# Optimization experiments

Hardware: AMD Instinct MI355X
Metric: run time of the kernel (lower is better)

## Reference

```python
import jax, jax.numpy as jnp
import numpy as np
from jax import lax

STRIDE = 1
PADDING = 1


def setup_inputs() -> dict:
    key = jax.random.key(0)
    k1, k2 = jax.random.split(key)
    x = jax.random.normal(k1, (32, 128, 56, 56), dtype=jnp.float32)
    weight = jax.random.normal(k2, (256, 128, 3, 3), dtype=jnp.float32)
    bias = jnp.zeros((256,), dtype=jnp.float32)
    return {"x": x, "weight": weight, "bias": bias}


def reference(x, weight, bias):
    # Standard 2D cross-correlation (the intended math of the torch
    # unfold + broadcast-multiply + sum implementation):
    #   out[b,o,h,w] = sum_{i,kh,kw} x_pad[b,i,h*s+kh,w*s+kw] * weight[o,i,kh,kw] + bias[o]
    out = lax.conv_general_dilated(
        x, weight,
        window_strides=(STRIDE, STRIDE),
        padding=[(PADDING, PADDING), (PADDING, PADDING)],
        dimension_numbers=("NCHW", "OIHW", "NCHW"),
    )
    return out + bias[None, :, None, None]
```

## Files before the change

kernel.cpp:

```cpp
#include <hip/hip_runtime.h>
#include <cstdint>
#include <cstddef>

#define NB    32
#define CI    128
#define CO    256
#define HW_   56
#define HP    58
#define KTOT  1152
#define NKT   36
#define MTOT  (NB * HW_ * HW_)

static constexpr size_t XP_ELEMS = (size_t)NB * HP * HP * CI;
static constexpr size_t WT_ELEMS = (size_t)CO * KTOT;
static constexpr size_t XP_BYTES = XP_ELEMS * 2;
static constexpr size_t WT_BYTES = WT_ELEMS * 2;

typedef __attribute__((ext_vector_type(8))) short bf16x8;
typedef __attribute__((ext_vector_type(4))) float f32x4;

__device__ __forceinline__ short f32_to_bf16(float f) {
  uint32_t u = __float_as_uint(f);
  uint32_t r = (u + 0x7FFFu + ((u >> 16) & 1u)) >> 16;
  return (short)r;
}

typedef __attribute__((address_space(3))) void       lds_void;
typedef const __attribute__((address_space(1))) void gbl_void;

__device__ __forceinline__ void gload16(const void* g, void* l) {
  __builtin_amdgcn_global_load_lds((gbl_void*)g, (lds_void*)l, 16, 0, 0);
}

__global__ void pad_convert(const float* __restrict__ x, short* __restrict__ xp,
                            const float* __restrict__ wt, short* __restrict__ wbT) {
  __shared__ float lds[CI][57];
  const int blk = blockIdx.x;
  const int hp  = blk % HP;
  const int nb  = blk / HP;
  const int tid = threadIdx.x;

  if (blk < 1152) {
    int idx = blk * 256 + tid;
    int c  = idx & 127;
    int t  = idx >> 7;
    int kw = t % 3;  int t2 = t / 3;
    int kh = t2 % 3; int o  = t2 / 3;
    wbT[idx] = f32_to_bf16(wt[(((size_t)o * CI + c) * 3 + kh) * 3 + kw]);
  }

  const bool interior = (hp >= 1 && hp <= HW_);
  if (interior) {
    const float* src = x + (size_t)nb * CI * HW_ * HW_ + (size_t)(hp - 1) * HW_;
    for (int t = tid; t < CI * HW_; t += 256) {
      int c = t / HW_, w = t - (t / HW_) * HW_;
      lds[c][w] = src[(size_t)c * HW_ * HW_ + w];
    }
  }
  __syncthreads();
  short* dst = xp + (size_t)(nb * HP + hp) * HP * CI;
  for (int t = tid; t < HP * CI / 4; t += 256) {
    const int wp = t >> 5;
    const int c4 = (t & 31) * 4;
    short4 s;
    if (interior && wp >= 1 && wp <= HW_) {
      s.x = f32_to_bf16(lds[c4 + 0][wp - 1]);
      s.y = f32_to_bf16(lds[c4 + 1][wp - 1]);
      s.z = f32_to_bf16(lds[c4 + 2][wp - 1]);
      s.w = f32_to_bf16(lds[c4 + 3][wp - 1]);
    } else {
      s.x = s.y = s.z = s.w = 0;
    }
    *(short4*)(dst + t * 4) = s;
  }
}

__device__ __forceinline__ int stage_aoff(int u) {
  const int tap = u >> 2;
  const int cq  = u & 3;
  const int kh  = tap / 3, kw = tap - kh * 3;
  return ((kh * HP + kw) * CI + cq * 32) * 2;
}

__global__ __launch_bounds__(256, 2) void conv_gemm(
    const short* __restrict__ xp, const short* __restrict__ wbT,
    const float* __restrict__ bias, float* __restrict__ out) {
  __shared__ __align__(16) char lds_[3 * 24576];

  const int tid = threadIdx.x;
  const int l   = tid & 63;
  const int wv  = tid >> 6;
  const int wm  = wv >> 1;
  const int wn  = wv & 1;

  const int bid = blockIdx.x;
  const int lin = (bid & 7) * 98 + (bid >> 3);
  const int mt  = lin >> 1;
  const int nt  = lin & 1;

  const int pcs = (((l & 3) ^ ((l >> 3) & 3)) << 4);
  const int srow = 16 * wv + (l >> 2);
  const char *aSrc0, *aSrc1, *aSrc2, *aSrc3;
  {
#pragma unroll
    for (int g = 0; g < 4; ++g) {
      int m  = mt * 256 + 64 * g + srow;
      int nb = m / 3136, hw = m - nb * 3136;
      int h = hw / HW_, w = hw - (hw / HW_) * HW_;
      const char* p = (const char*)xp + ((size_t)((nb * HP + h) * HP + w) * CI) * 2 + pcs;
      if (g == 0) aSrc0 = p; else if (g == 1) aSrc1 = p;
      else if (g == 2) aSrc2 = p; else aSrc3 = p;
    }
  }
  const char* bSrc0 = (const char*)wbT + (size_t)(nt * 128 +      srow) * KTOT * 2 + pcs;
  const char* bSrc1 = (const char*)wbT + (size_t)(nt * 128 + 64 + srow) * KTOT * 2 + pcs;

  const int lm   = l & 15;
  const int koff = (((l >> 4) ^ ((l >> 1) & 3)) << 4);
  const int raOff = (wm * 128 + lm) * 64 + koff;
  const int rbOff = (wn * 64 + lm) * 64 + koff;

  char* B0 = lds_;
  char* B1 = lds_ + 24576;
  char* B2 = lds_ + 49152;

#define STAGE(U, BUF)                                                        \
  {                                                                          \
    const int ao_ = stage_aoff(U);                                           \
    const int bo_ = (U) * 64;                                                \
    gload16(aSrc0 + ao_, (BUF) +         wv * 1024);                         \
    gload16(aSrc1 + ao_, (BUF) +  4096 + wv * 1024);                         \
    gload16(aSrc2 + ao_, (BUF) +  8192 + wv * 1024);                         \
    gload16(aSrc3 + ao_, (BUF) + 12288 + wv * 1024);                         \
    gload16(bSrc0 + bo_, (BUF) + 16384 + wv * 1024);                         \
    gload16(bSrc1 + bo_, (BUF) + 20480 + wv * 1024);                         \
  }

  f32x4 acc[8][4];
#pragma unroll
  for (int g = 0; g < 8; ++g)
#pragma unroll
    for (int h = 0; h < 4; ++h) acc[g][h] = {0.f, 0.f, 0.f, 0.f};

  STAGE(0, B0)
  STAGE(1, B1)
  asm volatile("s_waitcnt vmcnt(6)" ::: "memory");
  __builtin_amdgcn_s_barrier();
  __builtin_amdgcn_sched_barrier(0);

#define TILE_BODY(V, CUR, STG)                                               \
  {                                                                          \
    const int v_ = (V);                                                      \
    if (v_ + 2 < NKT) STAGE(v_ + 2, STG)                                     \
    bf16x8 af[8], bf[4];                                                     \
    _Pragma("unroll") for (int g = 0; g < 8; ++g)                            \
        af[g] = *(const bf16x8*)((CUR) + raOff + g * 1024);                  \
    _Pragma("unroll") for (int h = 0; h < 4; ++h)                            \
        bf[h] = *(const bf16x8*)((CUR) + 16384 + rbOff + h * 1024);          \
    __builtin_amdgcn_s_setprio(1);                                           \
    _Pragma("unroll") for (int g = 0; g < 8; ++g)                            \
      _Pragma("unroll") for (int h = 0; h < 4; ++h)                          \
        acc[g][h] = __builtin_amdgcn_mfma_f32_16x16x32_bf16(                 \
            bf[h], af[g], acc[g][h], 0, 0, 0);                               \
    __builtin_amdgcn_s_setprio(0);                                           \
    if (v_ < NKT - 1) {                                                      \
      if (v_ == NKT - 2) { asm volatile("s_waitcnt vmcnt(0)" ::: "memory"); }\
      else               { asm volatile("s_waitcnt vmcnt(6)" ::: "memory"); }\
      __builtin_amdgcn_s_barrier();                                          \
      __builtin_amdgcn_sched_barrier(0);                                     \
    }                                                                        \
  }

  for (int v3 = 0; v3 < NKT; v3 += 3) {
    TILE_BODY(v3 + 0, B0, B2)
    TILE_BODY(v3 + 1, B1, B0)
    TILE_BODY(v3 + 2, B2, B1)
  }
#undef TILE_BODY
#undef STAGE

  const int mBase = mt * 256 + wm * 128 + lm;
  const int ocB   = nt * 128 + wn * 64 + (l >> 4) * 4;
  float bv[4][4];
#pragma unroll
  for (int h = 0; h < 4; ++h)
#pragma unroll
    for (int j = 0; j < 4; ++j) bv[h][j] = bias[ocB + h * 16 + j];
#pragma unroll
  for (int g = 0; g < 8; ++g) {
    const int m  = mBase + g * 16;
    const int nb = m / 3136;
    const int hw = m - nb * 3136;
    float* op = out + (size_t)nb * CO * 3136 + hw;
#pragma unroll
    for (int h = 0; h < 4; ++h) {
      const int oc = ocB + h * 16;
#pragma unroll
      for (int j = 0; j < 4; ++j)
        op[(size_t)(oc + j) * 3136] = acc[g][h][j] + bv[h][j];
    }
  }
}

__global__ void conv_naive(const float* __restrict__ x, const float* __restrict__ wt,
                           const float* __restrict__ bias, float* __restrict__ out) {
  const int idx = blockIdx.x * 256 + threadIdx.x;
  if (idx >= NB * CO * 3136) return;
  const int w  = idx % HW_;
  const int h  = (idx / HW_) % HW_;
  const int oc = (idx / 3136) % CO;
  const int nb = idx / (3136 * CO);
  float s = bias[oc];
  for (int c = 0; c < CI; ++c)
    for (int kh = 0; kh < 3; ++kh) {
      const int ih = h + kh - 1;
      if (ih < 0 || ih >= HW_) continue;
      for (int kw = 0; kw < 3; ++kw) {
        const int iw = w + kw - 1;
        if (iw < 0 || iw >= HW_) continue;
        s += x[((size_t)(nb * CI + c) * HW_ + ih) * HW_ + iw] *
             wt[(((size_t)oc * CI + c) * 3 + kh) * 3 + kw];
      }
    }
  out[idx] = s;
}

extern "C" void kernel_launch(void* const* d_in, const int* in_sizes, int n_in,
                              void* d_out, int out_size, void* d_ws, size_t ws_size,
                              hipStream_t stream) {
  const float* x    = (const float*)d_in[0];
  const float* wt   = (const float*)d_in[1];
  const float* bias = (const float*)d_in[2];
  float* out        = (float*)d_out;

  if (ws_size < XP_BYTES + WT_BYTES) {
    conv_naive<<<(NB * CO * 3136 + 255) / 256, 256, 0, stream>>>(x, wt, bias, out);
    return;
  }

  short* xp  = (short*)d_ws;
  short* wbT = (short*)((char*)d_ws + XP_BYTES);

  pad_convert<<<NB * HP, 256, 0, stream>>>(x, xp, wt, wbT);
  conv_gemm<<<(MTOT / 256) * 2, 256, 0, stream>>>(xp, wbT, bias, out);
}
```

Measured before the change: 94.21 us.

## Enlarge conv GEMM block tile to 256x256 with 8 waves and split-phase staging

```diff
diff --git a/kernel.cpp b/kernel.cpp
--- a/kernel.cpp
+++ b/kernel.cpp
@@ -82,38 +82,35 @@
   return ((kh * HP + kw) * CI + cq * 32) * 2;
 }
 
-__global__ __launch_bounds__(256, 2) void conv_gemm(
+__global__ __launch_bounds__(512, 2) void conv_gemm(
     const short* __restrict__ xp, const short* __restrict__ wbT,
     const float* __restrict__ bias, float* __restrict__ out) {
-  __shared__ __align__(16) char lds_[3 * 24576];
+  __shared__ __align__(16) char lds_[3 * 32768];
 
   const int tid = threadIdx.x;
   const int l   = tid & 63;
   const int wv  = tid >> 6;
-  const int wm  = wv >> 1;
-  const int wn  = wv & 1;
+  const int wm  = wv >> 2;
+  const int wn  = wv & 3;
 
   const int bid = blockIdx.x;
-  const int lin = (bid & 7) * 98 + (bid >> 3);
-  const int mt  = lin >> 1;
-  const int nt  = lin & 1;
-
-  const int pcs = (((l & 3) ^ ((l >> 3) & 3)) << 4);
-  const int srow = 16 * wv + (l >> 2);
-  const char *aSrc0, *aSrc1, *aSrc2, *aSrc3;
+  const int mt  = (bid & 7) * 49 + (bid >> 3);
+
+  const int pcs  = (((tid & 3) ^ ((tid >> 3) & 3)) << 4);
+  const int srow = tid >> 2;
+  const char *aSrc0, *aSrc1;
   {
 #pragma unroll
-    for (int g = 0; g < 4; ++g) {
-      int m  = mt * 256 + 64 * g + srow;
+    for (int q = 0; q < 2; ++q) {
+      int m  = mt * 256 + 128 * q + srow;
       int nb = m / 3136, hw = m - nb * 3136;
       int h = hw / HW_, w = hw - (hw / HW_) * HW_;
       const char* p = (const char*)xp + ((size_t)((nb * HP + h) * HP + w) * CI) * 2 + pcs;
-      if (g == 0) aSrc0 = p; else if (g == 1) aSrc1 = p;
-      else if (g == 2) aSrc2 = p; else aSrc3 = p;
-    }
-  }
-  const char* bSrc0 = (const char*)wbT + (size_t)(nt * 128 +      srow) * KTOT * 2 + pcs;
-  const char* bSrc1 = (const char*)wbT + (size_t)(nt * 128 + 64 + srow) * KTOT * 2 + pcs;
+      if (q == 0) aSrc0 = p; else aSrc1 = p;
+    }
+  }
+  const char* bSrc0 = (const char*)wbT + (size_t)(      srow) * KTOT * 2 + pcs;
+  const char* bSrc1 = (const char*)wbT + (size_t)(128 + srow) * KTOT * 2 + pcs;
 
   const int lm   = l & 15;
   const int koff = (((l >> 4) ^ ((l >> 1) & 3)) << 4);
@@ -121,19 +118,20 @@
   const int rbOff = (wn * 64 + lm) * 64 + koff;
 
   char* B0 = lds_;
-  char* B1 = lds_ + 24576;
-  char* B2 = lds_ + 49152;
-
-#define STAGE(U, BUF)                                                        \
+  char* B1 = lds_ + 32768;
+  char* B2 = lds_ + 65536;
+
+#define STAGE_A(U, BUF)                                                      \
   {                                                                          \
     const int ao_ = stage_aoff(U);                                           \
+    gload16(aSrc0 + ao_, (BUF) +        wv * 1024);                          \
+    gload16(aSrc1 + ao_, (BUF) + 8192 + wv * 1024);                          \
+  }
+#define STAGE_B(U, BUF)                                                      \
+  {                                                                          \
     const int bo_ = (U) * 64;                                                \
-    gload16(aSrc0 + ao_, (BUF) +         wv * 1024);                         \
-    gload16(aSrc1 + ao_, (BUF) +  4096 + wv * 1024);                         \
-    gload16(aSrc2 + ao_, (BUF) +  8192 + wv * 1024);                         \
-    gload16(aSrc3 + ao_, (BUF) + 12288 + wv * 1024);                         \
     gload16(bSrc0 + bo_, (BUF) + 16384 + wv * 1024);                         \
-    gload16(bSrc1 + bo_, (BUF) + 20480 + wv * 1024);                         \
+    gload16(bSrc1 + bo_, (BUF) + 24576 + wv * 1024);                         \
   }
 
   f32x4 acc[8][4];
@@ -142,32 +140,55 @@
 #pragma unroll
     for (int h = 0; h < 4; ++h) acc[g][h] = {0.f, 0.f, 0.f, 0.f};
 
-  STAGE(0, B0)
-  STAGE(1, B1)
-  asm volatile("s_waitcnt vmcnt(6)" ::: "memory");
+  STAGE_A(0, B0) STAGE_B(0, B0)
+  STAGE_A(1, B1) STAGE_B(1, B1)
+  asm volatile("s_waitcnt vmcnt(4)" ::: "memory");
   __builtin_amdgcn_s_barrier();
   __builtin_amdgcn_sched_barrier(0);
 
 #define TILE_BODY(V, CUR, STG)                                               \
   {                                                                          \
     const int v_ = (V);                                                      \
-    if (v_ + 2 < NKT) STAGE(v_ + 2, STG)                                     \
-    bf16x8 af[8], bf[4];                                                     \
-    _Pragma("unroll") for (int g = 0; g < 8; ++g)                            \
-        af[g] = *(const bf16x8*)((CUR) + raOff + g * 1024);                  \
-    _Pragma("unroll") for (int h = 0; h < 4; ++h)                            \
-        bf[h] = *(const bf16x8*)((CUR) + 16384 + rbOff + h * 1024);          \
-    __builtin_amdgcn_s_setprio(1);                                           \
-    _Pragma("unroll") for (int g = 0; g < 8; ++g)                            \
+    bf16x8 bf[4];                                                            \
+                                         \
+    if (v_ + 2 < NKT) STAGE_A(v_ + 2, STG)                                   \
+    {                                                                        \
+      bf16x8 af[4];                                                          \
+      _Pragma("unroll") for (int g = 0; g < 4; ++g)                          \
+          af[g] = *(const bf16x8*)((CUR) + raOff + g * 1024);                \
       _Pragma("unroll") for (int h = 0; h < 4; ++h)                          \
-        acc[g][h] = __builtin_amdgcn_mfma_f32_16x16x32_bf16(                 \
-            bf[h], af[g], acc[g][h], 0, 0, 0);                               \
-    __builtin_amdgcn_s_setprio(0);                                           \
-    if (v_ < NKT - 1) {                                                      \
-      if (v_ == NKT - 2) { asm volatile("s_waitcnt vmcnt(0)" ::: "memory"); }\
-      else               { asm volatile("s_waitcnt vmcnt(6)" ::: "memory"); }\
-      __builtin_amdgcn_s_barrier();                                          \
-      __builtin_amdgcn_sched_barrier(0);                                     \
+          bf[h] = *(const bf16x8*)((CUR) + 16384 + rbOff + h * 1024);        \
+      __builtin_amdgcn_s_barrier();                                          \
+      asm volatile("s_waitcnt lgkmcnt(0)" ::: "memory");                     \
+      __builtin_amdgcn_sched_barrier(0);                                     \
+      __builtin_amdgcn_s_setprio(1);                                         \
+      _Pragma("unroll") for (int g = 0; g < 4; ++g)                          \
+        _Pragma("unroll") for (int h = 0; h < 4; ++h)                        \
+          acc[g][h] = __builtin_amdgcn_mfma_f32_16x16x32_bf16(               \
+              bf[h], af[g], acc[g][h], 0, 0, 0);                             \
+      __builtin_amdgcn_s_setprio(0);                                         \
+      __builtin_amdgcn_sched_barrier(0);                                     \
+      __builtin_amdgcn_s_barrier();                                          \
+    }                                                                        \
+                        \
+    if (v_ + 2 < NKT) STAGE_B(v_ + 2, STG)                                   \
+    {                                                                        \
+      bf16x8 af[4];                                                          \
+      _Pragma("unroll") for (int g = 0; g < 4; ++g)                          \
+          af[g] = *(const bf16x8*)((CUR) + raOff + 4096 + g * 1024);         \
+      __builtin_amdgcn_s_barrier();                                          \
+      asm volatile("s_waitcnt lgkmcnt(0)" ::: "memory");                     \
+      __builtin_amdgcn_sched_barrier(0);                                     \
+      __builtin_amdgcn_s_setprio(1);                                         \
+      _Pragma("unroll") for (int g = 0; g < 4; ++g)                          \
+        _Pragma("unroll") for (int h = 0; h < 4; ++h)                        \
+          acc[4 + g][h] = __builtin_amdgcn_mfma_f32_16x16x32_bf16(           \
+              bf[h], af[g], acc[4 + g][h], 0, 0, 0);                         \
+      __builtin_amdgcn_s_setprio(0);                                         \
+      __builtin_amdgcn_sched_barrier(0);                                     \
+      if (v_ < NKT - 2)       { asm volatile("s_waitcnt vmcnt(4)" ::: "memory"); } \
+      else if (v_ == NKT - 2) { asm volatile("s_waitcnt vmcnt(0)" ::: "memory"); } \
+      __builtin_amdgcn_s_barrier();                                          \
     }                                                                        \
   }
 
@@ -177,10 +198,11 @@
     TILE_BODY(v3 + 2, B2, B1)
   }
 #undef TILE_BODY
-#undef STAGE
+#undef STAGE_A
+#undef STAGE_B
 
   const int mBase = mt * 256 + wm * 128 + lm;
-  const int ocB   = nt * 128 + wn * 64 + (l >> 4) * 4;
+  const int ocB   = wn * 64 + (l >> 4) * 4;
   float bv[4][4];
 #pragma unroll
   for (int h = 0; h < 4; ++h)
@@ -242,5 +264,5 @@
   short* wbT = (short*)((char*)d_ws + XP_BYTES);
 
   pad_convert<<<NB * HP, 256, 0, stream>>>(x, xp, wt, wbT);
-  conv_gemm<<<(MTOT / 256) * 2, 256, 0, stream>>>(xp, wbT, bias, out);
-}
+  conv_gemm<<<MTOT / 256, 512, 0, stream>>>(xp, wbT, bias, out);
+}
```

After: 98.61 us. 1.05x slower.

## Switch to 32x32x16 MFMA and load weights directly into registers

Applied to the files above, without the earlier changes.

```diff
diff --git a/kernel.cpp b/kernel.cpp
--- a/kernel.cpp
+++ b/kernel.cpp
@@ -16,8 +16,8 @@
 static constexpr size_t XP_BYTES = XP_ELEMS * 2;
 static constexpr size_t WT_BYTES = WT_ELEMS * 2;
 
-typedef __attribute__((ext_vector_type(8))) short bf16x8;
-typedef __attribute__((ext_vector_type(4))) float f32x4;
+typedef __attribute__((ext_vector_type(8)))  short bf16x8;
+typedef __attribute__((ext_vector_type(16))) float f32x16;
 
 __device__ __forceinline__ short f32_to_bf16(float f) {
   uint32_t u = __float_as_uint(f);
@@ -85,7 +85,7 @@
 __global__ __launch_bounds__(256, 2) void conv_gemm(
     const short* __restrict__ xp, const short* __restrict__ wbT,
     const float* __restrict__ bias, float* __restrict__ out) {
-  __shared__ __align__(16) char lds_[3 * 24576];
+  __shared__ __align__(16) char lds_[3 * 16384];
 
   const int tid = threadIdx.x;
   const int l   = tid & 63;
@@ -98,7 +98,7 @@
   const int mt  = lin >> 1;
   const int nt  = lin & 1;
 
-  const int pcs = (((l & 3) ^ ((l >> 3) & 3)) << 4);
+  const int pcs  = (((l & 3) ^ ((l >> 3) & 3)) << 4);
   const int srow = 16 * wv + (l >> 2);
   const char *aSrc0, *aSrc1, *aSrc2, *aSrc3;
   {
@@ -112,92 +112,119 @@
       else if (g == 2) aSrc2 = p; else aSrc3 = p;
     }
   }
-  const char* bSrc0 = (const char*)wbT + (size_t)(nt * 128 +      srow) * KTOT * 2 + pcs;
-  const char* bSrc1 = (const char*)wbT + (size_t)(nt * 128 + 64 + srow) * KTOT * 2 + pcs;
-
-  const int lm   = l & 15;
-  const int koff = (((l >> 4) ^ ((l >> 1) & 3)) << 4);
-  const int raOff = (wm * 128 + lm) * 64 + koff;
-  const int rbOff = (wn * 64 + lm) * 64 + koff;
+
+  const char* bAddr0 = (const char*)wbT +
+      (size_t)(nt * 128 + wn * 64 + 0 * 32 + (l & 31)) * (KTOT * 2) + ((l >> 5) * 16);
+  const char* bAddr1 = (const char*)wbT +
+      (size_t)(nt * 128 + wn * 64 + 1 * 32 + (l & 31)) * (KTOT * 2) + ((l >> 5) * 16);
+
+  const int arow = (wm * 128 + (l & 31)) * 64;
+  int aOff[4][2];
+#pragma unroll
+  for (int g = 0; g < 4; ++g)
+#pragma unroll
+    for (int kh = 0; kh < 2; ++kh)
+      aOff[g][kh] = arow + g * 32 * 64 +
+                    ((((kh * 2) + (l >> 5)) ^ ((l >> 1) & 3)) << 4);
 
   char* B0 = lds_;
-  char* B1 = lds_ + 24576;
-  char* B2 = lds_ + 49152;
-
-#define STAGE(U, BUF)                                                        \
+  char* B1 = lds_ + 16384;
+  char* B2 = lds_ + 32768;
+
+#define STAGE_A(U, BUF)                                                      \
   {                                                                          \
     const int ao_ = stage_aoff(U);                                           \
-    const int bo_ = (U) * 64;                                                \
     gload16(aSrc0 + ao_, (BUF) +         wv * 1024);                         \
     gload16(aSrc1 + ao_, (BUF) +  4096 + wv * 1024);                         \
     gload16(aSrc2 + ao_, (BUF) +  8192 + wv * 1024);                         \
     gload16(aSrc3 + ao_, (BUF) + 12288 + wv * 1024);                         \
-    gload16(bSrc0 + bo_, (BUF) + 16384 + wv * 1024);                         \
-    gload16(bSrc1 + bo_, (BUF) + 20480 + wv * 1024);                         \
-  }
-
-  f32x4 acc[8][4];
-#pragma unroll
-  for (int g = 0; g < 8; ++g)
-#pragma unroll
-    for (int h = 0; h < 4; ++h) acc[g][h] = {0.f, 0.f, 0.f, 0.f};
-
-  STAGE(0, B0)
-  STAGE(1, B1)
-  asm volatile("s_waitcnt vmcnt(6)" ::: "memory");
+  }
+#define LOAD_B(U, BF)                                                        \
+  {                                                                          \
+    const int bo_ = (U) * 64;                                                \
+    BF[0][0] = *(const bf16x8*)(bAddr0 + bo_);                               \
+    BF[0][1] = *(const bf16x8*)(bAddr0 + bo_ + 32);                          \
+    BF[1][0] = *(const bf16x8*)(bAddr1 + bo_);                               \
+    BF[1][1] = *(const bf16x8*)(bAddr1 + bo_ + 32);                          \
+  }
+
+  f32x16 acc[4][2];
+#pragma unroll
+  for (int g = 0; g < 4; ++g)
+#pragma unroll
+    for (int h = 0; h < 2; ++h)
+#pragma unroll
+      for (int e = 0; e < 16; ++e) acc[g][h][e] = 0.f;
+
+  bf16x8 bfP[2][2], bfQ[2][2];
+
+  STAGE_A(0, B0)
+  STAGE_A(1, B1)
+  LOAD_B(0, bfP)
+  asm volatile("s_waitcnt vmcnt(0)" ::: "memory");
   __builtin_amdgcn_s_barrier();
   __builtin_amdgcn_sched_barrier(0);
 
-#define TILE_BODY(V, CUR, STG)                                               \
+#define TILE_BODY(V, CUR, STG, BFC, BFN)                                     \
   {                                                                          \
     const int v_ = (V);                                                      \
-    if (v_ + 2 < NKT) STAGE(v_ + 2, STG)                                     \
-    bf16x8 af[8], bf[4];                                                     \
-    _Pragma("unroll") for (int g = 0; g < 8; ++g)                            \
-        af[g] = *(const bf16x8*)((CUR) + raOff + g * 1024);                  \
-    _Pragma("unroll") for (int h = 0; h < 4; ++h)                            \
-        bf[h] = *(const bf16x8*)((CUR) + 16384 + rbOff + h * 1024);          \
+    if (v_ + 1 < NKT) LOAD_B(v_ + 1, BFN)                                    \
+    if (v_ + 2 < NKT) STAGE_A(v_ + 2, STG)                                   \
+    bf16x8 af[4][2];                                                         \
+    _Pragma("unroll") for (int g = 0; g < 4; ++g)                            \
+      _Pragma("unroll") for (int kh = 0; kh < 2; ++kh)                       \
+        af[g][kh] = *(const bf16x8*)((CUR) + aOff[g][kh]);                   \
     __builtin_amdgcn_s_setprio(1);                                           \
-    _Pragma("unroll") for (int g = 0; g < 8; ++g)                            \
-      _Pragma("unroll") for (int h = 0; h < 4; ++h)                          \
-        acc[g][h] = __builtin_amdgcn_mfma_f32_16x16x32_bf16(                 \
-            bf[h], af[g], acc[g][h], 0, 0, 0);                               \
+    _Pragma("unroll") for (int kh = 0; kh < 2; ++kh)                         \
+      _Pragma("unroll") for (int g = 0; g < 4; ++g)                          \
+        _Pragma("unroll") for (int h = 0; h < 2; ++h)                        \
+          acc[g][h] = __builtin_amdgcn_mfma_f32_32x32x16_bf16(               \
+              BFC[h][kh], af[g][kh], acc[g][h], 0, 0, 0);                    \
     __builtin_amdgcn_s_setprio(0);                                           \
     if (v_ < NKT - 1) {                                                      \
-      if (v_ == NKT - 2) { asm volatile("s_waitcnt vmcnt(0)" ::: "memory"); }\
-      else               { asm volatile("s_waitcnt vmcnt(6)" ::: "memory"); }\
+      if (v_ >= NKT - 3) { asm volatile("s_waitcnt vmcnt(0)" ::: "memory"); }\
+      else               { asm volatile("s_waitcnt vmcnt(4)" ::: "memory"); }\
       __builtin_amdgcn_s_barrier();                                          \
       __builtin_amdgcn_sched_barrier(0);                                     \
     }                                                                        \
   }
 
-  for (int v3 = 0; v3 < NKT; v3 += 3) {
-    TILE_BODY(v3 + 0, B0, B2)
-    TILE_BODY(v3 + 1, B1, B0)
-    TILE_BODY(v3 + 2, B2, B1)
+  for (int v6 = 0; v6 < NKT; v6 += 6) {
+    TILE_BODY(v6 + 0, B0, B2, bfP, bfQ)
+    TILE_BODY(v6 + 1, B1, B0, bfQ, bfP)
+    TILE_BODY(v6 + 2, B2, B1, bfP, bfQ)
+    TILE_BODY(v6 + 3, B0, B2, bfQ, bfP)
+    TILE_BODY(v6 + 4, B1, B0, bfP, bfQ)
+    TILE_BODY(v6 + 5, B2, B1, bfQ, bfP)
   }
 #undef TILE_BODY
-#undef STAGE
-
-  const int mBase = mt * 256 + wm * 128 + lm;
-  const int ocB   = nt * 128 + wn * 64 + (l >> 4) * 4;
-  float bv[4][4];
-#pragma unroll
-  for (int h = 0; h < 4; ++h)
-#pragma unroll
-    for (int j = 0; j < 4; ++j) bv[h][j] = bias[ocB + h * 16 + j];
-#pragma unroll
-  for (int g = 0; g < 8; ++g) {
-    const int m  = mBase + g * 16;
-    const int nb = m / 3136;
-    const int hw = m - nb * 3136;
+#undef STAGE_A
+#undef LOAD_B
+
+  const int ocB = nt * 128 + wn * 64 + 4 * (l >> 5);
+  float bb[2][16];
+#pragma unroll
+  for (int h = 0; h < 2; ++h)
+#pragma unroll
+    for (int q = 0; q < 4; ++q)
+#pragma unroll
+      for (int j = 0; j < 4; ++j)
+        bb[h][q * 4 + j] = bias[ocB + h * 32 + q * 8 + j];
+#pragma unroll
+  for (int g = 0; g < 4; ++g) {
+    const int mB = mt * 256 + wm * 128 + g * 32;
+    const int nb = mB / 3136;
+    const int hw = mB - nb * 3136 + (l & 31);
     float* op = out + (size_t)nb * CO * 3136 + hw;
 #pragma unroll
-    for (int h = 0; h < 4; ++h) {
-      const int oc = ocB + h * 16;
-#pragma unroll
-      for (int j = 0; j < 4; ++j)
-        op[(size_t)(oc + j) * 3136] = acc[g][h][j] + bv[h][j];
+    for (int h = 0; h < 2; ++h) {
+#pragma unroll
+      for (int q = 0; q < 4; ++q)
+#pragma unroll
+        for (int j = 0; j < 4; ++j) {
+          const int oc = ocB + h * 32 + q * 8 + j;
+          op[(size_t)oc * 3136] = acc[g][h][q * 4 + j] + bb[h][q * 4 + j];
+        }
     }
   }
 }
```

New measurement: 132.1 us. 1.4x slower.

## Prepack weights in MFMA fragment order and load B directly to registers

Applied to the files above, without the earlier changes.

```diff
diff --git a/kernel.cpp b/kernel.cpp
--- a/kernel.cpp
+++ b/kernel.cpp
@@ -17,6 +17,7 @@
 static constexpr size_t WT_BYTES = WT_ELEMS * 2;
 
 typedef __attribute__((ext_vector_type(8))) short bf16x8;
+typedef __attribute__((ext_vector_type(8))) short short8v;
 typedef __attribute__((ext_vector_type(4))) float f32x4;
 
 __device__ __forceinline__ short f32_to_bf16(float f) {
@@ -33,20 +34,27 @@
 }
 
 __global__ void pad_convert(const float* __restrict__ x, short* __restrict__ xp,
-                            const float* __restrict__ wt, short* __restrict__ wbT) {
+                            const float* __restrict__ wt, short* __restrict__ wbF) {
   __shared__ float lds[CI][57];
   const int blk = blockIdx.x;
   const int hp  = blk % HP;
   const int nb  = blk / HP;
   const int tid = threadIdx.x;
 
-  if (blk < 1152) {
-    int idx = blk * 256 + tid;
-    int c  = idx & 127;
-    int t  = idx >> 7;
-    int kw = t % 3;  int t2 = t / 3;
-    int kh = t2 % 3; int o  = t2 / 3;
-    wbT[idx] = f32_to_bf16(wt[(((size_t)o * CI + c) * 3 + kh) * 3 + kw]);
+  if (blk < 144) {
+    const int idx = blk * 256 + tid;
+    const int lam = idx & 63;
+    const int v   = (idx >> 6) % NKT;
+    const int g2  = idx / (64 * NKT);
+    const int oc  = g2 * 16 + (lam & 15);
+    const int tap = v >> 2;
+    const int kh  = tap / 3, kw = tap - kh * 3;
+    const int c0  = (v & 3) * 32 + (lam >> 4) * 8;
+    short8v s;
+#pragma unroll
+    for (int j = 0; j < 8; ++j)
+      s[j] = f32_to_bf16(wt[(((size_t)oc * CI + c0 + j) * 3 + kh) * 3 + kw]);
+    *(short8v*)(wbF + (size_t)idx * 8) = s;
   }
 
   const bool interior = (hp >= 1 && hp <= HW_);
@@ -83,9 +91,9 @@
 }
 
 __global__ __launch_bounds__(256, 2) void conv_gemm(
-    const short* __restrict__ xp, const short* __restrict__ wbT,
+    const short* __restrict__ xp, const short* __restrict__ wbF,
     const float* __restrict__ bias, float* __restrict__ out) {
-  __shared__ __align__(16) char lds_[3 * 24576];
+  __shared__ __align__(16) char lds_[3 * 16384];
 
   const int tid = threadIdx.x;
   const int l   = tid & 63;
@@ -98,7 +106,7 @@
   const int mt  = lin >> 1;
   const int nt  = lin & 1;
 
-  const int pcs = (((l & 3) ^ ((l >> 3) & 3)) << 4);
+  const int pcs  = (((l & 3) ^ ((l >> 3) & 3)) << 4);
   const int srow = 16 * wv + (l >> 2);
   const char *aSrc0, *aSrc1, *aSrc2, *aSrc3;
   {
@@ -112,28 +120,35 @@
       else if (g == 2) aSrc2 = p; else aSrc3 = p;
     }
   }
-  const char* bSrc0 = (const char*)wbT + (size_t)(nt * 128 +      srow) * KTOT * 2 + pcs;
-  const char* bSrc1 = (const char*)wbT + (size_t)(nt * 128 + 64 + srow) * KTOT * 2 + pcs;
+
+  const char* bAddr0 = (const char*)wbF + ((size_t)((nt * 8 + wn * 4 + 0) * NKT) * 64 + l) * 16;
+  const char* bAddr1 = (const char*)wbF + ((size_t)((nt * 8 + wn * 4 + 1) * NKT) * 64 + l) * 16;
+  const char* bAddr2 = (const char*)wbF + ((size_t)((nt * 8 + wn * 4 + 2) * NKT) * 64 + l) * 16;
+  const char* bAddr3 = (const char*)wbF + ((size_t)((nt * 8 + wn * 4 + 3) * NKT) * 64 + l) * 16;
 
   const int lm   = l & 15;
   const int koff = (((l >> 4) ^ ((l >> 1) & 3)) << 4);
   const int raOff = (wm * 128 + lm) * 64 + koff;
-  const int rbOff = (wn * 64 + lm) * 64 + koff;
 
   char* B0 = lds_;
-  char* B1 = lds_ + 24576;
-  char* B2 = lds_ + 49152;
-
-#define STAGE(U, BUF)                                                        \
+  char* B1 = lds_ + 16384;
+  char* B2 = lds_ + 32768;
+
+#define STAGE_A(U, BUF)                                                      \
   {                                                                          \
     const int ao_ = stage_aoff(U);                                           \
-    const int bo_ = (U) * 64;                                                \
     gload16(aSrc0 + ao_, (BUF) +         wv * 1024);                         \
     gload16(aSrc1 + ao_, (BUF) +  4096 + wv * 1024);                         \
     gload16(aSrc2 + ao_, (BUF) +  8192 + wv * 1024);                         \
     gload16(aSrc3 + ao_, (BUF) + 12288 + wv * 1024);                         \
-    gload16(bSrc0 + bo_, (BUF) + 16384 + wv * 1024);                         \
-    gload16(bSrc1 + bo_, (BUF) + 20480 + wv * 1024);                         \
+  }
+#define LOAD_B(U, BF)                                                        \
+  {                                                                          \
+    const size_t bo_ = (size_t)(U) * 1024;                                   \
+    BF[0] = *(const bf16x8*)(bAddr0 + bo_);                                  \
+    BF[1] = *(const bf16x8*)(bAddr1 + bo_);                                  \
+    BF[2] = *(const bf16x8*)(bAddr2 + bo_);                                  \
+    BF[3] = *(const bf16x8*)(bAddr3 + bo_);                                  \
   }
 
   f32x4 acc[8][4];
@@ -142,42 +157,47 @@
 #pragma unroll
     for (int h = 0; h < 4; ++h) acc[g][h] = {0.f, 0.f, 0.f, 0.f};
 
-  STAGE(0, B0)
-  STAGE(1, B1)
-  asm volatile("s_waitcnt vmcnt(6)" ::: "memory");
+  bf16x8 bfP[4], bfQ[4];
+
+  STAGE_A(0, B0)
+  STAGE_A(1, B1)
+  LOAD_B(0, bfP)
+  asm volatile("s_waitcnt vmcnt(8)" ::: "memory");
   __builtin_amdgcn_s_barrier();
   __builtin_amdgcn_sched_barrier(0);
 
-#define TILE_BODY(V, CUR, STG)                                               \
+#define TILE_BODY(V, CUR, STG, BFC, BFN)                                     \
   {                                                                          \
     const int v_ = (V);                                                      \
-    if (v_ + 2 < NKT) STAGE(v_ + 2, STG)                                     \
-    bf16x8 af[8], bf[4];                                                     \
+    if (v_ + 1 < NKT) LOAD_B(v_ + 1, BFN)                                    \
+    if (v_ + 2 < NKT) STAGE_A(v_ + 2, STG)                                   \
+    bf16x8 af[8];                                                            \
     _Pragma("unroll") for (int g = 0; g < 8; ++g)                            \
         af[g] = *(const bf16x8*)((CUR) + raOff + g * 1024);                  \
-    _Pragma("unroll") for (int h = 0; h < 4; ++h)                            \
-        bf[h] = *(const bf16x8*)((CUR) + 16384 + rbOff + h * 1024);          \
     __builtin_amdgcn_s_setprio(1);                                           \
     _Pragma("unroll") for (int g = 0; g < 8; ++g)                            \
       _Pragma("unroll") for (int h = 0; h < 4; ++h)                          \
         acc[g][h] = __builtin_amdgcn_mfma_f32_16x16x32_bf16(                 \
-            bf[h], af[g], acc[g][h], 0, 0, 0);                               \
+            BFC[h], af[g], acc[g][h], 0, 0, 0);                              \
     __builtin_amdgcn_s_setprio(0);                                           \
     if (v_ < NKT - 1) {                                                      \
-      if (v_ == NKT - 2) { asm volatile("s_waitcnt vmcnt(0)" ::: "memory"); }\
-      else               { asm volatile("s_waitcnt vmcnt(6)" ::: "memory"); }\
+      asm volatile("s_waitcnt vmcnt(4)" ::: "memory");                       \
       __builtin_amdgcn_s_barrier();                                          \
       __builtin_amdgcn_sched_barrier(0);                                     \
     }                                                                        \
   }
 
-  for (int v3 = 0; v3 < NKT; v3 += 3) {
-    TILE_BODY(v3 + 0, B0, B2)
-    TILE_BODY(v3 + 1, B1, B0)
-    TILE_BODY(v3 + 2, B2, B1)
+  for (int v6 = 0; v6 < NKT; v6 += 6) {
+    TILE_BODY(v6 + 0, B0, B2, bfP, bfQ)
+    TILE_BODY(v6 + 1, B1, B0, bfQ, bfP)
+    TILE_BODY(v6 + 2, B2, B1, bfP, bfQ)
+    TILE_BODY(v6 + 3, B0, B2, bfQ, bfP)
+    TILE_BODY(v6 + 4, B1, B0, bfP, bfQ)
+    TILE_BODY(v6 + 5, B2, B1, bfQ, bfP)
   }
 #undef TILE_BODY
-#undef STAGE
+#undef STAGE_A
+#undef LOAD_B
 
   const int mBase = mt * 256 + wm * 128 + lm;
   const int ocB   = nt * 128 + wn * 64 + (l >> 4) * 4;
@@ -239,8 +259,8 @@
   }
 
   short* xp  = (short*)d_ws;
-  short* wbT = (short*)((char*)d_ws + XP_BYTES);
-
-  pad_convert<<<NB * HP, 256, 0, stream>>>(x, xp, wt, wbT);
-  conv_gemm<<<(MTOT / 256) * 2, 256, 0, stream>>>(xp, wbT, bias, out);
-}
+  short* wbF = (short*)((char*)d_ws + XP_BYTES);
+
+  pad_convert<<<NB * HP, 256, 0, stream>>>(x, xp, wt, wbF);
+  conv_gemm<<<(MTOT / 256) * 2, 256, 0, stream>>>(xp, wbF, bias, out);
+}
```

Result: slower. 142.5 us (+51.2%).
